# Kernel tuning notes

Hardware: AMD Instinct MI355X
Metric: run time of the kernel (lower is better)

The kernel has to match this reference:

```python
import jax, jax.numpy as jnp
import numpy as np

B, S, DIM, H, HD = 2, 2048, 512, 8, 64
VD = DIM // H  # 64
QK = H * HD


def setup_inputs() -> dict:
    key = jax.random.key(0)
    k1, k2, k3, k4, k5 = jax.random.split(key, 5)
    x = jax.random.normal(k1, (B, S, DIM), dtype=jnp.float32)
    mask = jax.random.bernoulli(k2, 0.5, (B, S))
    # per-position rotation matrices, scaled to keep activations O(1)
    rotator = jax.random.normal(k3, (B, S, HD, HD), dtype=jnp.float32) / np.sqrt(HD)
    # torch Linear weights: [out_features, in_features], no bias
    W_trans = jax.random.normal(k4, (2 * QK + DIM, DIM), dtype=jnp.float32) / np.sqrt(DIM)
    W_o = jax.random.normal(k5, (DIM, DIM), dtype=jnp.float32) / np.sqrt(DIM)
    return {"x": x, "mask": mask, "rotator": rotator, "W_trans": W_trans, "W_o": W_o}


def _taylor_attention(qs, ks, vs, mask):
    # 2nd-order Taylor approximation of exp for softmax weights
    # qs/ks: [B,S,H,HD], vs: [B,S,H,VD], mask: [B,S] key mask
    scores = jnp.einsum('bqhd,bkhd->bhqk', qs, ks) / np.sqrt(HD)
    w = 1.0 + scores + 0.5 * scores * scores
    w = jnp.where(mask[:, None, None, :], w, 0.0)
    w = w / jnp.sum(w, axis=-1, keepdims=True)
    out = jnp.einsum('bhqk,bkhd->bqhd', w, vs)
    return out.reshape(out.shape[0], out.shape[1], -1)  # [B,S,DIM]


def reference(x, mask, rotator, W_trans, W_o):
    t = x @ W_trans.T  # [B,S,2*QK+DIM]
    qs = t[..., :QK].reshape(B, S, H, HD)
    ks = t[..., QK:2 * QK].reshape(B, S, H, HD)
    vs = t[..., 2 * QK:].reshape(B, S, H, VD)
    sel = mask[..., None, None]
    qs = jnp.where(sel, jnp.einsum('bsij,bshj->bshi', rotator, qs), qs)
    ks = jnp.where(sel, jnp.einsum('bsij,bshj->bshi', rotator, ks), ks)
    out = _taylor_attention(qs, ks, vs, mask)
    return out @ W_o.T
```

## Files before the change

kernel.cpp:

```cpp
#include <hip/hip_runtime.h>
#include <hip/hip_bf16.h>

#define B_    2
#define S_    2048
#define DIM_  512
#define H_    8
#define HD_   64
#define TOUT_ 1536
#define ROWS_ (B_ * S_)

typedef unsigned short ushort_t;
typedef __attribute__((ext_vector_type(8))) __bf16 bf16x8;
typedef __attribute__((ext_vector_type(4))) float floatx4;

#define AS_GLB __attribute__((address_space(1)))
#define AS_LDS __attribute__((address_space(3)))

__device__ __forceinline__ float bf2f(unsigned int u) { return __uint_as_float(u << 16); }
__device__ __forceinline__ unsigned short f2bfu(float f) {
    unsigned u = __float_as_uint(f);
    unsigned r = (u + 0x7fffu + ((u >> 16) & 1u)) >> 16;
    return (unsigned short)r;
}
__device__ __forceinline__ bf16x8 cvt8(const float* p) {
    float4 a = *reinterpret_cast<const float4*>(p);
    float4 b = *reinterpret_cast<const float4*>(p + 4);
    ushort_t o[8] = {f2bfu(a.x), f2bfu(a.y), f2bfu(a.z), f2bfu(a.w),
                     f2bfu(b.x), f2bfu(b.y), f2bfu(b.z), f2bfu(b.w)};
    return *reinterpret_cast<bf16x8*>(o);
}

__global__ void tmha_detect(const unsigned char* mb, int* flags) {
    __shared__ int s_bf, s_f, s_u8;
    int tid = threadIdx.x;
    if (tid == 0) { s_bf = 0; s_f = 0; s_u8 = 0; }
    __syncthreads();
    int cbf = 0, cf = 0, cu8 = 0;
    for (int i = tid; i < 4096; i += 256) {
        unsigned char v = mb[i];
        if (v == 0x3F || v == 0x80) {
            cf++;
            if ((i & 3) == 1) cbf++;
        } else if (v != 0 && (i & 3) != 0) {
            cu8++;
        }
    }
    atomicAdd(&s_bf, cbf); atomicAdd(&s_f, cf); atomicAdd(&s_u8, cu8);
    __syncthreads();
    if (tid == 0) {
        int mcls;
        if (s_bf > 0)      mcls = 2;
        else if (s_f > 0)  mcls = 3;
        else if (s_u8 > 0) mcls = 0;
        else               mcls = 1;
        flags[1] = mcls;
    }
}

__global__ void tmha_decode_mask(const unsigned char* mb, const int* flags, int* wm) {
    int i = blockIdx.x * 256 + threadIdx.x;
    if (i >= ROWS_) return;
    int cls = flags[1];
    int v;
    if (cls == 0)      v = (mb[i] != 0);
    else if (cls == 1) v = (reinterpret_cast<const int*>(mb)[i] != 0);
    else if (cls == 2) v = ((reinterpret_cast<const unsigned short*>(mb)[i] & 0x7fffu) != 0);
    else               v = ((reinterpret_cast<const unsigned int*>(mb)[i] & 0x7fffffffu) != 0);
    wm[i] = v;
}

__global__ __launch_bounds__(256) void cast_bf16(const float* __restrict__ src,
                                                 ushort_t* __restrict__ dst, int n4) {
    int i = blockIdx.x * 256 + threadIdx.x;
    if (i >= n4) return;
    float4 v = reinterpret_cast<const float4*>(src)[i];
    ushort_t o[4] = {f2bfu(v.x), f2bfu(v.y), f2bfu(v.z), f2bfu(v.w)};
    reinterpret_cast<uint2*>(dst)[i] = *reinterpret_cast<uint2*>(o);
}

template <int TM, int N, int K>
__global__ __launch_bounds__(256) void mfma_gemm_bt(const ushort_t* __restrict__ A,
                                                    const ushort_t* __restrict__ Bm,
                                                    float* __restrict__ C) {
    constexpr int FM = TM / 32;
    __shared__ __align__(16) ushort_t As[TM * 64];
    __shared__ __align__(16) ushort_t Bs[128 * 64];
    int tid = threadIdx.x;
    int lane = tid & 63;
    int wv = tid >> 6;
    int wm = wv >> 1, wn = wv & 1;
    int quad = lane >> 4;
    int mrow = lane & 15;
    int bx = blockIdx.x;
    int by = blockIdx.y;

    floatx4 acc[FM][4];
#pragma unroll
    for (int i = 0; i < FM; i++)
#pragma unroll
        for (int j = 0; j < 4; j++) acc[i][j] = (floatx4){0.f, 0.f, 0.f, 0.f};

    for (int k0 = 0; k0 < K; k0 += 64) {
#pragma unroll
        for (int t = 0; t < TM / 32; t++) {
            int p = (wv * (TM / 32) + t) * 64 + lane;
            int row = p >> 3, cp = p & 7;
            int gc = cp ^ (row & 7);
            const ushort_t* ga = A + (size_t)(by * TM + row) * K + k0 + gc * 8;
            __builtin_amdgcn_global_load_lds((const AS_GLB unsigned int*)ga,
                                             (AS_LDS unsigned int*)&As[(size_t)(wv * (TM / 32) + t) * 64 * 8],
                                             16, 0, 0);
        }
#pragma unroll
        for (int t = 0; t < 4; t++) {
            int p = (wv * 4 + t) * 64 + lane;
            int row = p >> 3, cp = p & 7;
            int gc = cp ^ (row & 7);
            const ushort_t* gb = Bm + (size_t)(bx * 128 + row) * K + k0 + gc * 8;
            __builtin_amdgcn_global_load_lds((const AS_GLB unsigned int*)gb,
                                             (AS_LDS unsigned int*)&Bs[(size_t)(wv * 4 + t) * 64 * 8],
                                             16, 0, 0);
        }
        __syncthreads();
#pragma unroll
        for (int ks = 0; ks < 64; ks += 32) {
            int c = (ks >> 3) + quad;
            bf16x8 af[FM], bf[4];
#pragma unroll
            for (int i = 0; i < FM; i++) {
                int row = wm * (TM / 2) + i * 16 + mrow;
                int pos = row * 8 + (c ^ (row & 7));
                af[i] = *reinterpret_cast<const bf16x8*>(&As[pos * 8]);
            }
#pragma unroll
            for (int j = 0; j < 4; j++) {
                int row = wn * 64 + j * 16 + mrow;
                int pos = row * 8 + (c ^ (row & 7));
                bf[j] = *reinterpret_cast<const bf16x8*>(&Bs[pos * 8]);
            }
#pragma unroll
            for (int i = 0; i < FM; i++)
#pragma unroll
                for (int j = 0; j < 4; j++)
                    acc[i][j] = __builtin_amdgcn_mfma_f32_16x16x32_bf16(af[i], bf[j], acc[i][j], 0, 0, 0);
        }
        __syncthreads();
    }

    int col0 = bx * 128 + wn * 64 + mrow;
    int row0 = by * TM + wm * (TM / 2) + quad * 4;
#pragma unroll
    for (int i = 0; i < FM; i++)
#pragma unroll
        for (int j = 0; j < 4; j++)
#pragma unroll
            for (int r = 0; r < 4; r++)
                C[(size_t)(row0 + i * 16 + r) * N + col0 + j * 16] = acc[i][j][r];
}

__global__ __launch_bounds__(256) void rot_qk_mfma(const float* __restrict__ t,
                                                   const float* __restrict__ rotG,
                                                   const int* __restrict__ wm,
                                                   ushort_t* __restrict__ Qb,
                                                   ushort_t* __restrict__ Kb) {
    int lane = threadIdx.x & 63;
    int wv = threadIdx.x >> 6;
    int row = blockIdx.x * 4 + wv;
    int b = row >> 11, s = row & 2047;
    int lm = lane & 15, quad = lane >> 4;
    const float* trow = t + (size_t)row * TOUT_;

    if (wm[row]) {
        bf16x8 af[2];
#pragma unroll
        for (int kc = 0; kc < 2; kc++)
            af[kc] = cvt8(trow + lm * 64 + kc * 32 + quad * 8);

        const float* R = rotG + (size_t)row * 4096;
        floatx4 dacc[4];
#pragma unroll
        for (int nb = 0; nb < 4; nb++) dacc[nb] = (floatx4){0.f, 0.f, 0.f, 0.f};
#pragma unroll
        for (int nb = 0; nb < 4; nb++)
#pragma unroll
            for (int kc = 0; kc < 2; kc++) {
                bf16x8 bfr = cvt8(R + (size_t)(nb * 16 + lm) * 64 + kc * 32 + quad * 8);
                dacc[nb] = __builtin_amdgcn_mfma_f32_16x16x32_bf16(af[kc], bfr, dacc[nb], 0, 0, 0);
            }
#pragma unroll
        for (int nb = 0; nb < 4; nb++)
#pragma unroll
            for (int r = 0; r < 4; r++) {
                int vec = quad * 4 + r;
                int h = vec & 7;
                ushort_t* dst = (vec >= 8 ? Kb : Qb);
                dst[((size_t)(b * 8 + h) * 2048 + s) * 64 + nb * 16 + lm] = f2bfu(dacc[nb][r]);
            }
    } else {
#pragma unroll
        for (int nb = 0; nb < 4; nb++)
#pragma unroll
            for (int r = 0; r < 4; r++) {
                int vec = quad * 4 + r;
                int h = vec & 7;
                float v = trow[vec * 64 + nb * 16 + lm];
                ushort_t* dst = (vec >= 8 ? Kb : Qb);
                dst[((size_t)(b * 8 + h) * 2048 + s) * 64 + nb * 16 + lm] = f2bfu(v);
            }
    }
}

__global__ __launch_bounds__(256) void prep_vt(const float* __restrict__ t,
                                               const int* __restrict__ wm,
                                               ushort_t* __restrict__ VtG) {
    __shared__ float tile[64][65];
    __shared__ float mrow[64];
    int st = blockIdx.x;
    int bh = blockIdx.y;
    int b = bh >> 3, h = bh & 7;
    int tid = threadIdx.x;
    if (tid < 64) mrow[tid] = wm[b * 2048 + st * 64 + tid] ? 1.0f : 0.0f;
#pragma unroll
    for (int i = 0; i < 4; i++) {
        int q = i * 256 + tid;
        int r = q >> 4, c4 = (q & 15) * 4;
        float4 v = *reinterpret_cast<const float4*>(
            t + (size_t)(b * 2048 + st * 64 + r) * TOUT_ + 1024 + h * 64 + c4);
        tile[r][c4] = v.x; tile[r][c4 + 1] = v.y; tile[r][c4 + 2] = v.z; tile[r][c4 + 3] = v.w;
    }
    __syncthreads();
#pragma unroll
    for (int i = 0; i < 8; i++) {
        int e = i * 256 + tid;
        int d = e >> 5, sl = (e & 31) * 2;
        float v0 = tile[sl][d] * mrow[sl];
        float v1 = tile[sl + 1][d] * mrow[sl + 1];
        unsigned int u = (unsigned)f2bfu(v0) | ((unsigned)f2bfu(v1) << 16);
        *reinterpret_cast<unsigned int*>(VtG + ((size_t)bh * 65 + d) * 2048 + st * 64 + sl) = u;
    }
    if (tid < 32) {
        int sl = tid * 2;
        unsigned m0 = mrow[sl]     != 0.f ? 0x3F80u : 0u;
        unsigned m1 = mrow[sl + 1] != 0.f ? 0x3F80u : 0u;
        *reinterpret_cast<unsigned int*>(VtG + ((size_t)bh * 65 + 64) * 2048 + st * 64 + sl) = m0 | (m1 << 16);
    }
}

__global__ __launch_bounds__(256) void tmha_attn_mfma(const ushort_t* __restrict__ Qb,
                                                      const ushort_t* __restrict__ Kb,
                                                      const ushort_t* __restrict__ VtG,
                                                      float* __restrict__ numer,
                                                      float* __restrict__ den) {
    __shared__ __align__(16) ushort_t Ks[1024 * 8];
    __shared__ __align__(16) ushort_t Vs[1280 * 8];
    __shared__ __align__(16) ushort_t Ps[1024 * 8];
    int tid = threadIdx.x;
    int lane = tid & 63;
    int wv = tid >> 6;
    int lm = lane & 15;
    int quad = lane >> 4;
    int qt = blockIdx.x;
    int h = blockIdx.y;
    int z = blockIdx.z;
    int b = z >> 1;
    int ks = z & 1;
    int bh = b * 8 + h;

    for (int i = tid; i < 960; i += 256)
        reinterpret_cast<unsigned int*>(&Vs[1040 * 8])[i] = 0u;

    bf16x8 qf[2];
    {
        const ushort_t* qp = Qb + ((size_t)bh * 2048 + qt * 64 + wv * 16 + lm) * 64 + quad * 8;
        qf[0] = *reinterpret_cast<const bf16x8*>(qp);
        qf[1] = *reinterpret_cast<const bf16x8*>(qp + 32);
    }

    floatx4 oacc[5];
#pragma unroll
    for (int j = 0; j < 5; j++) oacc[j] = (floatx4){0.f, 0.f, 0.f, 0.f};

    for (int kt = ks * 1024; kt < ks * 1024 + 1024; kt += 128) {
#pragma unroll
        for (int t4 = 0; t4 < 4; t4++) {
            int p = (wv * 4 + t4) * 64 + lane;
            int row = p >> 3, cp = p & 7;
            int gc = cp ^ (row & 7);
            const ushort_t* g = Kb + ((size_t)bh * 2048 + kt + row) * 64 + gc * 8;
            __builtin_amdgcn_global_load_lds((const AS_GLB unsigned int*)g,
                                             (AS_LDS unsigned int*)&Ks[(size_t)(wv * 4 + t4) * 64 * 8],
                                             16, 0, 0);
        }
#pragma unroll
        for (int t4 = 0; t4 < 4; t4++) {
            int p = (wv * 4 + t4) * 64 + lane;
            int row = p >> 4, cp = p & 15;
            int gc = cp ^ (row & 15);
            const ushort_t* g = VtG + ((size_t)bh * 65 + row) * 2048 + kt + gc * 8;
            __builtin_amdgcn_global_load_lds((const AS_GLB unsigned int*)g,
                                             (AS_LDS unsigned int*)&Vs[(size_t)(wv * 4 + t4) * 64 * 8],
                                             16, 0, 0);
        }
        if (tid < 64) {
            unsigned int mv = *reinterpret_cast<const unsigned int*>(
                VtG + ((size_t)bh * 65 + 64) * 2048 + kt + tid * 2);
            reinterpret_cast<unsigned int*>(&Vs[1024 * 8])[tid] = mv;
        }
        __syncthreads();

        floatx4 sacc[8];
#pragma unroll
        for (int j = 0; j < 8; j++) sacc[j] = (floatx4){0.f, 0.f, 0.f, 0.f};
#pragma unroll
        for (int j = 0; j < 8; j++) {
            int row = j * 16 + lm;
#pragma unroll
            for (int kc = 0; kc < 2; kc++) {
                int c = kc * 4 + quad;
                int pos = row * 8 + (c ^ (row & 7));
                bf16x8 bk = *reinterpret_cast<const bf16x8*>(&Ks[pos * 8]);
                sacc[j] = __builtin_amdgcn_mfma_f32_16x16x32_bf16(qf[kc], bk, sacc[j], 0, 0, 0);
            }
        }

#pragma unroll
        for (int j = 0; j < 8; j++)
#pragma unroll
            for (int r = 0; r < 4; r++) {
                float s = sacc[j][r];
                float wgt = fmaf(s, fmaf(s, 0.0078125f, 0.125f), 1.0f);
                int m = wv * 16 + quad * 4 + r;
                int col = j * 16 + lm;
                int cw = col >> 3;
                int pos = m * 16 + (cw ^ (m & 15));
                Ps[pos * 8 + (col & 7)] = f2bfu(wgt);
            }
        __syncthreads();

#pragma unroll
        for (int j = 0; j < 5; j++) {
            int vrow = j * 16 + lm;
#pragma unroll
            for (int kc = 0; kc < 4; kc++) {
                int c = kc * 4 + quad;
                int ppos = (wv * 16 + lm) * 16 + (c ^ lm);
                bf16x8 pa = *reinterpret_cast<const bf16x8*>(&Ps[ppos * 8]);
                int vpos = vrow * 16 + (c ^ (vrow & 15));
                bf16x8 vb = *reinterpret_cast<const bf16x8*>(&Vs[vpos * 8]);
                oacc[j] = __builtin_amdgcn_mfma_f32_16x16x32_bf16(pa, vb, oacc[j], 0, 0, 0);
            }
        }
        __syncthreads();
    }

#pragma unroll
    for (int j = 0; j < 4; j++)
#pragma unroll
        for (int r = 0; r < 4; r++) {
            int qrow = b * 2048 + qt * 64 + wv * 16 + quad * 4 + r;
            numer[((size_t)ks * ROWS_ + qrow) * DIM_ + h * 64 + j * 16 + lm] = oacc[j][r];
        }
    if (lm == 0) {
#pragma unroll
        for (int r = 0; r < 4; r++) {
            int qrow = b * 2048 + qt * 64 + wv * 16 + quad * 4 + r;
            den[((size_t)ks * ROWS_ + qrow) * 8 + h] = oacc[4][r];
        }
    }
}

__global__ __launch_bounds__(256) void attn_combine(const float* __restrict__ numer,
                                                    const float* __restrict__ den,
                                                    ushort_t* __restrict__ attnAb) {
    int i = blockIdx.x * 256 + threadIdx.x;
    int row = i >> 7;
    int c4 = (i & 127) * 4;
    int h = c4 >> 6;
    float4 n0 = *reinterpret_cast<const float4*>(&numer[(size_t)row * DIM_ + c4]);
    float4 n1 = *reinterpret_cast<const float4*>(&numer[((size_t)ROWS_ + row) * DIM_ + c4]);
    float d = den[(size_t)row * 8 + h] + den[((size_t)ROWS_ + row) * 8 + h];
    float inv = 1.0f / d;
    ushort_t o[4] = {f2bfu((n0.x + n1.x) * inv), f2bfu((n0.y + n1.y) * inv),
                     f2bfu((n0.z + n1.z) * inv), f2bfu((n0.w + n1.w) * inv)};
    *reinterpret_cast<uint2*>(&attnAb[(size_t)row * DIM_ + c4]) = *reinterpret_cast<uint2*>(o);
}

extern "C" void kernel_launch(void* const* d_in, const int* in_sizes, int n_in,
                              void* d_out, int out_size, void* d_ws, size_t ws_size,
                              hipStream_t stream) {
    (void)in_sizes; (void)n_in; (void)out_size; (void)ws_size;
    const float* x    = (const float*)d_in[0];
    const void*  mask = d_in[1];
    const float* rot  = (const float*)d_in[2];
    const float* Wt   = (const float*)d_in[3];
    const float* Wo   = (const float*)d_in[4];

    char* ws = (char*)d_ws;
    int* flags       = (int*)ws;
    int* wmask       = (int*)(ws + 64);
    float* t         = (float*)(ws + 32768);
    ushort_t* Xb     = (ushort_t*)(ws + 25198592);
    ushort_t* Wtb    = (ushort_t*)(ws + 29392896);
    ushort_t* Wob    = (ushort_t*)(ws + 30965760);
    ushort_t* Qb     = (ushort_t*)(ws + 31490048);
    ushort_t* Kb     = (ushort_t*)(ws + 35684352);
    ushort_t* VtG    = (ushort_t*)(ws + 39878656);
    ushort_t* attnAb = (ushort_t*)(ws + 44138496);
    float* numer     = t;
    float* den       = (float*)(ws + 32768 + 16777216);

    tmha_detect<<<1, 256, 0, stream>>>((const unsigned char*)mask, flags);
    tmha_decode_mask<<<16, 256, 0, stream>>>((const unsigned char*)mask, flags, wmask);

    cast_bf16<<<(ROWS_ * DIM_ / 4 + 255) / 256, 256, 0, stream>>>(x, Xb, ROWS_ * DIM_ / 4);
    cast_bf16<<<(TOUT_ * DIM_ / 4 + 255) / 256, 256, 0, stream>>>(Wt, Wtb, TOUT_ * DIM_ / 4);
    cast_bf16<<<(DIM_ * DIM_ / 4 + 255) / 256, 256, 0, stream>>>(Wo, Wob, DIM_ * DIM_ / 4);

    {
        dim3 grid(TOUT_ / 128, ROWS_ / 64);
        mfma_gemm_bt<64, TOUT_, DIM_><<<grid, 256, 0, stream>>>(Xb, Wtb, t);
    }

    rot_qk_mfma<<<ROWS_ / 4, 256, 0, stream>>>(t, rot, wmask, Qb, Kb);

    {
        dim3 grid(32, 16);
        prep_vt<<<grid, 256, 0, stream>>>(t, wmask, VtG);
    }

    {
        dim3 grid(32, 8, 4);
        tmha_attn_mfma<<<grid, 256, 0, stream>>>(Qb, Kb, VtG, numer, den);
    }
    attn_combine<<<(ROWS_ * 128) / 256, 256, 0, stream>>>(numer, den, attnAb);

    {
        dim3 grid(DIM_ / 128, ROWS_ / 64);
        mfma_gemm_bt<64, DIM_, DIM_><<<grid, 256, 0, stream>>>(attnAb, Wob, (float*)d_out);
    }
}
```

Before: 200.3 us.

## Rework attention kernel onto 32x32x16 MFMA with 2x2 wave split over query/key

Rewrites the Taylor attention kernel to use 32x32x16 bf16 MFMA tiles. The four waves are split into two query groups and two key halves per 128-key tile, the V mask row moves into a separate small LDS buffer, and padding is replaced by a zero buffer. Each key half writes its own partial numerator and denominator, so the combine kernel now sums four partials stored in new workspace regions. The aim is fewer MFMA issues and less LDS fragment traffic, with a launch bound of 3 blocks per CU. The cost is more partial-output memory traffic and higher register pressure from the floatx16 accumulators.

```diff
diff --git a/kernel.cpp b/kernel.cpp
--- a/kernel.cpp
+++ b/kernel.cpp
@@ -12,21 +12,21 @@
 typedef unsigned short ushort_t;
 typedef __attribute__((ext_vector_type(8))) __bf16 bf16x8;
 typedef __attribute__((ext_vector_type(4))) float floatx4;
+typedef __attribute__((ext_vector_type(16))) float floatx16;
 
 #define AS_GLB __attribute__((address_space(1)))
 #define AS_LDS __attribute__((address_space(3)))
 
 __device__ __forceinline__ float bf2f(unsigned int u) { return __uint_as_float(u << 16); }
-__device__ __forceinline__ unsigned short f2bfu(float f) {
+__device__ __forceinline__ unsigned int f2bfu(float f) {
     unsigned u = __float_as_uint(f);
-    unsigned r = (u + 0x7fffu + ((u >> 16) & 1u)) >> 16;
-    return (unsigned short)r;
+    return (u + 0x7fffu + ((u >> 16) & 1u)) >> 16;
 }
 __device__ __forceinline__ bf16x8 cvt8(const float* p) {
     float4 a = *reinterpret_cast<const float4*>(p);
     float4 b = *reinterpret_cast<const float4*>(p + 4);
-    ushort_t o[8] = {f2bfu(a.x), f2bfu(a.y), f2bfu(a.z), f2bfu(a.w),
-                     f2bfu(b.x), f2bfu(b.y), f2bfu(b.z), f2bfu(b.w)};
+    ushort_t o[8] = {(ushort_t)f2bfu(a.x), (ushort_t)f2bfu(a.y), (ushort_t)f2bfu(a.z), (ushort_t)f2bfu(a.w),
+                     (ushort_t)f2bfu(b.x), (ushort_t)f2bfu(b.y), (ushort_t)f2bfu(b.z), (ushort_t)f2bfu(b.w)};
     return *reinterpret_cast<bf16x8*>(o);
 }
 
@@ -74,7 +74,7 @@
     int i = blockIdx.x * 256 + threadIdx.x;
     if (i >= n4) return;
     float4 v = reinterpret_cast<const float4*>(src)[i];
-    ushort_t o[4] = {f2bfu(v.x), f2bfu(v.y), f2bfu(v.z), f2bfu(v.w)};
+    ushort_t o[4] = {(ushort_t)f2bfu(v.x), (ushort_t)f2bfu(v.y), (ushort_t)f2bfu(v.z), (ushort_t)f2bfu(v.w)};
     reinterpret_cast<uint2*>(dst)[i] = *reinterpret_cast<uint2*>(o);
 }
 
@@ -194,7 +194,7 @@
                 int vec = quad * 4 + r;
                 int h = vec & 7;
                 ushort_t* dst = (vec >= 8 ? Kb : Qb);
-                dst[((size_t)(b * 8 + h) * 2048 + s) * 64 + nb * 16 + lm] = f2bfu(dacc[nb][r]);
+                dst[((size_t)(b * 8 + h) * 2048 + s) * 64 + nb * 16 + lm] = (ushort_t)f2bfu(dacc[nb][r]);
             }
     } else {
 #pragma unroll
@@ -205,7 +205,7 @@
                 int h = vec & 7;
                 float v = trow[vec * 64 + nb * 16 + lm];
                 ushort_t* dst = (vec >= 8 ? Kb : Qb);
-                dst[((size_t)(b * 8 + h) * 2048 + s) * 64 + nb * 16 + lm] = f2bfu(v);
+                dst[((size_t)(b * 8 + h) * 2048 + s) * 64 + nb * 16 + lm] = (ushort_t)f2bfu(v);
             }
     }
 }
@@ -235,7 +235,7 @@
         int d = e >> 5, sl = (e & 31) * 2;
         float v0 = tile[sl][d] * mrow[sl];
         float v1 = tile[sl + 1][d] * mrow[sl + 1];
-        unsigned int u = (unsigned)f2bfu(v0) | ((unsigned)f2bfu(v1) << 16);
+        unsigned int u = f2bfu(v0) | (f2bfu(v1) << 16);
         *reinterpret_cast<unsigned int*>(VtG + ((size_t)bh * 65 + d) * 2048 + st * 64 + sl) = u;
     }
     if (tid < 32) {
@@ -246,39 +246,44 @@
     }
 }
 
-__global__ __launch_bounds__(256) void tmha_attn_mfma(const ushort_t* __restrict__ Qb,
-                                                      const ushort_t* __restrict__ Kb,
-                                                      const ushort_t* __restrict__ VtG,
-                                                      float* __restrict__ numer,
-                                                      float* __restrict__ den) {
-    __shared__ __align__(16) ushort_t Ks[1024 * 8];
-    __shared__ __align__(16) ushort_t Vs[1280 * 8];
-    __shared__ __align__(16) ushort_t Ps[1024 * 8];
+__global__ __launch_bounds__(256, 3) void tmha_attn_mfma(const ushort_t* __restrict__ Qb,
+                                                         const ushort_t* __restrict__ Kb,
+                                                         const ushort_t* __restrict__ VtG,
+                                                         float* __restrict__ numer,
+                                                         float* __restrict__ den) {
+    __shared__ __align__(16) ushort_t Ks[128 * 64];
+    __shared__ __align__(16) ushort_t Vs[64 * 128];
+    __shared__ __align__(16) ushort_t Ps[64 * 128];
+    __shared__ __align__(16) ushort_t Ms[128];
+    __shared__ __align__(16) ushort_t Zb[8];
     int tid = threadIdx.x;
     int lane = tid & 63;
     int wv = tid >> 6;
-    int lm = lane & 15;
-    int quad = lane >> 4;
+    int qg = wv >> 1, kg = wv & 1;
+    int l31 = lane & 31, lhi = lane >> 5;
     int qt = blockIdx.x;
     int h = blockIdx.y;
     int z = blockIdx.z;
-    int b = z >> 1;
-    int ks = z & 1;
+    int b = z >> 1, ks = z & 1;
     int bh = b * 8 + h;
-
-    for (int i = tid; i < 960; i += 256)
-        reinterpret_cast<unsigned int*>(&Vs[1040 * 8])[i] = 0u;
-
-    bf16x8 qf[2];
+    if (tid < 4) reinterpret_cast<unsigned int*>(Zb)[tid] = 0u;
+
+    bf16x8 qf[4];
     {
-        const ushort_t* qp = Qb + ((size_t)bh * 2048 + qt * 64 + wv * 16 + lm) * 64 + quad * 8;
+        const ushort_t* qp = Qb + ((size_t)bh * 2048 + qt * 64 + qg * 32 + l31) * 64 + lhi * 8;
         qf[0] = *reinterpret_cast<const bf16x8*>(qp);
-        qf[1] = *reinterpret_cast<const bf16x8*>(qp + 32);
-    }
-
-    floatx4 oacc[5];
-#pragma unroll
-    for (int j = 0; j < 5; j++) oacc[j] = (floatx4){0.f, 0.f, 0.f, 0.f};
+        qf[1] = *reinterpret_cast<const bf16x8*>(qp + 16);
+        qf[2] = *reinterpret_cast<const bf16x8*>(qp + 32);
+        qf[3] = *reinterpret_cast<const bf16x8*>(qp + 48);
+    }
+
+    floatx16 oacc[3];
+#pragma unroll
+    for (int nt = 0; nt < 3; nt++)
+#pragma unroll
+        for (int e = 0; e < 16; e++) oacc[nt][e] = 0.f;
+
+    int q = qg * 32 + l31;
 
     for (int kt = ks * 1024; kt < ks * 1024 + 1024; kt += 128) {
 #pragma unroll
@@ -302,70 +307,86 @@
                                              16, 0, 0);
         }
         if (tid < 64) {
-            unsigned int mv = *reinterpret_cast<const unsigned int*>(
+            reinterpret_cast<unsigned int*>(Ms)[tid] = *reinterpret_cast<const unsigned int*>(
                 VtG + ((size_t)bh * 65 + 64) * 2048 + kt + tid * 2);
-            reinterpret_cast<unsigned int*>(&Vs[1024 * 8])[tid] = mv;
         }
         __syncthreads();
 
-        floatx4 sacc[8];
-#pragma unroll
-        for (int j = 0; j < 8; j++) sacc[j] = (floatx4){0.f, 0.f, 0.f, 0.f};
-#pragma unroll
-        for (int j = 0; j < 8; j++) {
-            int row = j * 16 + lm;
-#pragma unroll
-            for (int kc = 0; kc < 2; kc++) {
-                int c = kc * 4 + quad;
-                int pos = row * 8 + (c ^ (row & 7));
-                bf16x8 bk = *reinterpret_cast<const bf16x8*>(&Ks[pos * 8]);
-                sacc[j] = __builtin_amdgcn_mfma_f32_16x16x32_bf16(qf[kc], bk, sacc[j], 0, 0, 0);
-            }
-        }
-
-#pragma unroll
-        for (int j = 0; j < 8; j++)
+        floatx16 sacc[2];
+#pragma unroll
+        for (int mt = 0; mt < 2; mt++)
+#pragma unroll
+            for (int e = 0; e < 16; e++) sacc[mt][e] = 0.f;
+#pragma unroll
+        for (int kstep = 0; kstep < 4; kstep++) {
+            int g = kstep * 2 + lhi;
+#pragma unroll
+            for (int mt = 0; mt < 2; mt++) {
+                int row = kg * 64 + mt * 32 + l31;
+                int pos = row * 8 + (g ^ (row & 7));
+                bf16x8 kf = *reinterpret_cast<const bf16x8*>(&Ks[pos * 8]);
+                sacc[mt] = __builtin_amdgcn_mfma_f32_32x32x16_bf16(kf, qf[kstep], sacc[mt], 0, 0, 0);
+            }
+        }
+
+#pragma unroll
+        for (int mt = 0; mt < 2; mt++)
+#pragma unroll
+            for (int gg = 0; gg < 4; gg++) {
+                float w[4];
+#pragma unroll
+                for (int r = 0; r < 4; r++) {
+                    float s = sacc[mt][gg * 4 + r];
+                    w[r] = fmaf(s, fmaf(s, 0.0078125f, 0.125f), 1.0f);
+                }
+                int k0 = kg * 64 + mt * 32 + gg * 8 + lhi * 4;
+                int g16 = k0 >> 3;
+                int pos = q * 16 + (g16 ^ (q & 15));
+                uint2 u;
+                u.x = f2bfu(w[0]) | (f2bfu(w[1]) << 16);
+                u.y = f2bfu(w[2]) | (f2bfu(w[3]) << 16);
+                *reinterpret_cast<uint2*>(&Ps[pos * 8 + (k0 & 7)]) = u;
+            }
+        __syncthreads();
+
+#pragma unroll
+        for (int kstep = 0; kstep < 4; kstep++) {
+            int gk = kg * 8 + kstep * 2 + lhi;
+            int ppos = q * 16 + (gk ^ (q & 15));
+            bf16x8 pa = *reinterpret_cast<const bf16x8*>(&Ps[ppos * 8]);
+#pragma unroll
+            for (int nt = 0; nt < 3; nt++) {
+                int vrow = nt * 32 + l31;
+                const ushort_t* vp;
+                if (vrow < 64)       vp = &Vs[(vrow * 16 + (gk ^ (vrow & 15))) * 8];
+                else if (vrow == 64) vp = &Ms[gk * 8];
+                else                 vp = Zb;
+                bf16x8 vb = *reinterpret_cast<const bf16x8*>(vp);
+                oacc[nt] = __builtin_amdgcn_mfma_f32_32x32x16_bf16(pa, vb, oacc[nt], 0, 0, 0);
+            }
+        }
+        __syncthreads();
+    }
+
+    int sidx = ks * 2 + kg;
+    int qbase = b * 2048 + qt * 64 + qg * 32;
+#pragma unroll
+    for (int nt = 0; nt < 2; nt++)
+#pragma unroll
+        for (int gg = 0; gg < 4; gg++)
 #pragma unroll
             for (int r = 0; r < 4; r++) {
-                float s = sacc[j][r];
-                float wgt = fmaf(s, fmaf(s, 0.0078125f, 0.125f), 1.0f);
-                int m = wv * 16 + quad * 4 + r;
-                int col = j * 16 + lm;
-                int cw = col >> 3;
-                int pos = m * 16 + (cw ^ (m & 15));
-                Ps[pos * 8 + (col & 7)] = f2bfu(wgt);
-            }
-        __syncthreads();
-
-#pragma unroll
-        for (int j = 0; j < 5; j++) {
-            int vrow = j * 16 + lm;
-#pragma unroll
-            for (int kc = 0; kc < 4; kc++) {
-                int c = kc * 4 + quad;
-                int ppos = (wv * 16 + lm) * 16 + (c ^ lm);
-                bf16x8 pa = *reinterpret_cast<const bf16x8*>(&Ps[ppos * 8]);
-                int vpos = vrow * 16 + (c ^ (vrow & 15));
-                bf16x8 vb = *reinterpret_cast<const bf16x8*>(&Vs[vpos * 8]);
-                oacc[j] = __builtin_amdgcn_mfma_f32_16x16x32_bf16(pa, vb, oacc[j], 0, 0, 0);
-            }
-        }
-        __syncthreads();
-    }
-
-#pragma unroll
-    for (int j = 0; j < 4; j++)
-#pragma unroll
-        for (int r = 0; r < 4; r++) {
-            int qrow = b * 2048 + qt * 64 + wv * 16 + quad * 4 + r;
-            numer[((size_t)ks * ROWS_ + qrow) * DIM_ + h * 64 + j * 16 + lm] = oacc[j][r];
-        }
-    if (lm == 0) {
-#pragma unroll
-        for (int r = 0; r < 4; r++) {
-            int qrow = b * 2048 + qt * 64 + wv * 16 + quad * 4 + r;
-            den[((size_t)ks * ROWS_ + qrow) * 8 + h] = oacc[4][r];
-        }
+                int qrow = qbase + r + 8 * gg + 4 * lhi;
+                numer[((size_t)sidx * ROWS_ + qrow) * DIM_ + h * 64 + nt * 32 + l31] = oacc[nt][gg * 4 + r];
+            }
+    if (l31 == 0) {
+#pragma unroll
+        for (int gg = 0; gg < 4; gg++)
+#pragma unroll
+            for (int r = 0; r < 4; r++) {
+                int qrow = qbase + r + 8 * gg + 4 * lhi;
+                den[((size_t)sidx * ROWS_ + qrow) * 8 + h] = oacc[2][gg * 4 + r];
+            }
     }
 }
 
@@ -376,12 +397,16 @@
     int row = i >> 7;
     int c4 = (i & 127) * 4;
     int h = c4 >> 6;
-    float4 n0 = *reinterpret_cast<const float4*>(&numer[(size_t)row * DIM_ + c4]);
-    float4 n1 = *reinterpret_cast<const float4*>(&numer[((size_t)ROWS_ + row) * DIM_ + c4]);
-    float d = den[(size_t)row * 8 + h] + den[((size_t)ROWS_ + row) * 8 + h];
+    float nx = 0.f, ny = 0.f, nz = 0.f, nw = 0.f, d = 0.f;
+#pragma unroll
+    for (int s = 0; s < 4; s++) {
+        float4 n = *reinterpret_cast<const float4*>(&numer[((size_t)s * ROWS_ + row) * DIM_ + c4]);
+        nx += n.x; ny += n.y; nz += n.z; nw += n.w;
+        d += den[((size_t)s * ROWS_ + row) * 8 + h];
+    }
     float inv = 1.0f / d;
-    ushort_t o[4] = {f2bfu((n0.x + n1.x) * inv), f2bfu((n0.y + n1.y) * inv),
-                     f2bfu((n0.z + n1.z) * inv), f2bfu((n0.w + n1.w) * inv)};
+    ushort_t o[4] = {(ushort_t)f2bfu(nx * inv), (ushort_t)f2bfu(ny * inv),
+                     (ushort_t)f2bfu(nz * inv), (ushort_t)f2bfu(nw * inv)};
     *reinterpret_cast<uint2*>(&attnAb[(size_t)row * DIM_ + c4]) = *reinterpret_cast<uint2*>(o);
 }
 
@@ -406,8 +431,8 @@
     ushort_t* Kb     = (ushort_t*)(ws + 35684352);
     ushort_t* VtG    = (ushort_t*)(ws + 39878656);
     ushort_t* attnAb = (ushort_t*)(ws + 44138496);
-    float* numer     = t;
-    float* den       = (float*)(ws + 32768 + 16777216);
+    float* numer     = (float*)(ws + 50331648);
+    float* den       = (float*)(ws + 83886080);
 
     tmha_detect<<<1, 256, 0, stream>>>((const unsigned char*)mask, flags);
     tmha_decode_mask<<<16, 256, 0, stream>>>((const unsigned char*)mask, flags, wmask);
```

Result: no change. 202.7 us (+1.2%).
